# Kernel tuning notes

Measured on AMD Instinct MI355X. Metric: run time of the kernel, lower is better.

## Reference

```python
import jax, jax.numpy as jnp
import numpy as np

CLIP_MIN = -3.5
CLIP_MAX = 3.5
ALPHA = 0.25


def setup_inputs() -> dict:
    key = jax.random.key(0)
    x = jax.random.normal(key, (64, 2048, 256), dtype=jnp.float32)
    return {"x": x}


def reference(x):
    # clamp, then exponential moving average along time (dim 1)
    xc = jnp.clip(x, CLIP_MIN, CLIP_MAX)          # [B, T, F]
    x0 = xc[:, 0]                                  # [B, F] -> smoothed[0] = x[0]

    def step(carry, xt):
        s = ALPHA * xt + (1.0 - ALPHA) * carry
        return s, s

    # scan over time: inputs [T-1, B, F]
    _, rest = jax.lax.scan(step, x0, jnp.moveaxis(xc[:, 1:], 1, 0))
    smoothed = jnp.concatenate([x0[:, None], jnp.moveaxis(rest, 0, 1)], axis=1)
    return smoothed
```

## Files before the change

kernel.cpp:

```cpp
#include <hip/hip_runtime.h>


constexpr int B = 64;
constexpr int T = 2048;
constexpr int C = 256;
constexpr int L = 256;
constexpr int W = 64;
constexpr int NCHUNK = T / L;

#define EMA_ALPHA 0.25f
#define EMA_BETA  0.75f

__device__ __forceinline__ float clipf(float v) {
    return fminf(fmaxf(v, -3.5f), 3.5f);
}

__global__ __launch_bounds__(256, 2) void ema_chunk_kernel(
    const float* __restrict__ x, float* __restrict__ out)
{
    const int b  = blockIdx.x / NCHUNK;
    const int k  = blockIdx.x % NCHUNK;
    const int c  = threadIdx.x;
    const int t0 = k * L;

    int idx;
    float s;

    if (k == 0) {
        idx = b * T * C + c;
        s = clipf(x[idx]);
    } else {
        idx = (b * T + (t0 - W)) * C + c;
        s = clipf(x[idx]);
#pragma unroll 8
        for (int i = 0; i < W; ++i) {
            idx += C;
            float v = clipf(x[idx]);
            s = fmaf(EMA_ALPHA, v, EMA_BETA * s);
        }
    }

    out[idx] = s;
#pragma unroll 8
    for (int i = 1; i < L; ++i) {
        idx += C;
        float v = clipf(x[idx]);
        s = fmaf(EMA_ALPHA, v, EMA_BETA * s);
        out[idx] = s;
    }
}

extern "C" void kernel_launch(void* const* d_in, const int* in_sizes, int n_in,
                              void* d_out, int out_size, void* d_ws, size_t ws_size,
                              hipStream_t stream) {
    const float* x = (const float*)d_in[0];
    float* out = (float*)d_out;
    ema_chunk_kernel<<<dim3(B * NCHUNK), dim3(256), 0, stream>>>(x, out);
}
```

Before: 246.8 us.

## Shorten EMA chunks, vectorize channels as float2, use nontemporal stores

Cuts the time chunk length from 256 to 32 and the warm-up window from 64 to 24, so there are many more independent sequential jobs. Each half-block now handles one job, with 128 lanes each processing two channels through float2 loads. Outputs are written with nontemporal stores, and launch bounds now allow more resident blocks. This is meant to hide memory latency in the serial scan through much higher occupancy. The cost is extra warm-up reads, about 75% more input traffic, and a larger truncation error from the shorter warm-up (0.75^24 is about 1e-3), which may break tolerance.

```diff
diff --git a/kernel.cpp b/kernel.cpp
--- a/kernel.cpp
+++ b/kernel.cpp
@@ -4,9 +4,11 @@
 constexpr int B = 64;
 constexpr int T = 2048;
 constexpr int C = 256;
-constexpr int L = 256;
-constexpr int W = 64;
+constexpr int L = 32;
+constexpr int W = 24;
 constexpr int NCHUNK = T / L;
+constexpr int LANES = C / 2;
+constexpr int ROWF2 = C / 2;
 
 #define EMA_ALPHA 0.25f
 #define EMA_BETA  0.75f
@@ -15,38 +17,54 @@
     return fminf(fmaxf(v, -3.5f), 3.5f);
 }
 
-__global__ __launch_bounds__(256, 2) void ema_chunk_kernel(
+__device__ __forceinline__ float2 clip2(float2 v) {
+    return make_float2(clipf(v.x), clipf(v.y));
+}
+
+__device__ __forceinline__ void nt_store2(float2* p, float2 v) {
+    union { float2 f2; unsigned long long u; } u;
+    u.f2 = v;
+    __builtin_nontemporal_store(u.u, (unsigned long long*)p);
+}
+
+__global__ __launch_bounds__(256, 8) void ema_kernel(
     const float* __restrict__ x, float* __restrict__ out)
 {
-    const int b  = blockIdx.x / NCHUNK;
-    const int k  = blockIdx.x % NCHUNK;
-    const int c  = threadIdx.x;
-    const int t0 = k * L;
+    const int job  = blockIdx.x * 2 + (threadIdx.x >> 7);
+    const int lane = threadIdx.x & (LANES - 1);
+    const int b    = job >> 6;
+    const int k    = job & (NCHUNK - 1);
+    const int t0   = k * L;
+
+    const float2* __restrict__ xin = (const float2*)x;
+    float2* __restrict__ o         = (float2*)out;
 
     int idx;
-    float s;
+    float2 s;
 
     if (k == 0) {
-        idx = b * T * C + c;
-        s = clipf(x[idx]);
+        idx = (b * T) * ROWF2 + lane;
+        s = clip2(xin[idx]);
     } else {
-        idx = (b * T + (t0 - W)) * C + c;
-        s = clipf(x[idx]);
+        idx = (b * T + (t0 - W)) * ROWF2 + lane;
+        s = clip2(xin[idx]);
 #pragma unroll 8
         for (int i = 0; i < W; ++i) {
-            idx += C;
-            float v = clipf(x[idx]);
-            s = fmaf(EMA_ALPHA, v, EMA_BETA * s);
+            idx += ROWF2;
+            float2 v = clip2(xin[idx]);
+            s.x = fmaf(EMA_ALPHA, v.x, EMA_BETA * s.x);
+            s.y = fmaf(EMA_ALPHA, v.y, EMA_BETA * s.y);
         }
     }
 
-    out[idx] = s;
+    nt_store2(&o[idx], s);
 #pragma unroll 8
     for (int i = 1; i < L; ++i) {
-        idx += C;
-        float v = clipf(x[idx]);
-        s = fmaf(EMA_ALPHA, v, EMA_BETA * s);
-        out[idx] = s;
+        idx += ROWF2;
+        float2 v = clip2(xin[idx]);
+        s.x = fmaf(EMA_ALPHA, v.x, EMA_BETA * s.x);
+        s.y = fmaf(EMA_ALPHA, v.y, EMA_BETA * s.y);
+        nt_store2(&o[idx], s);
     }
 }
 
@@ -55,5 +73,6 @@
                               hipStream_t stream) {
     const float* x = (const float*)d_in[0];
     float* out = (float*)d_out;
-    ema_chunk_kernel<<<dim3(B * NCHUNK), dim3(256), 0, stream>>>(x, out);
+    const int n_jobs = B * NCHUNK;
+    ema_kernel<<<dim3(n_jobs / 2), dim3(256), 0, stream>>>(x, out);
 }
```

Result: faster. 236.0 us (-4.4%).
